# Kernel tuning notes

Measured on AMD Instinct MI355X. Metric: run time of the kernel, lower is better.

## Reference

```python
import jax, jax.numpy as jnp
import numpy as np

NUM_HEADS = 16

def setup_inputs() -> dict:
    key = jax.random.key(0)
    ks = jax.random.split(key, 6)
    B, N, E = 2, 2048, 2048
    QK, V, M = 2048, 2048, 4096
    x = jax.random.normal(ks[0], (B, N, E), dtype=jnp.float32)
    Wq = jax.random.normal(ks[1], (QK, E), dtype=jnp.float32) * 0.02
    k_weight = jax.random.normal(ks[2], (M, QK), dtype=jnp.float32) * 0.05
    v_weight = jax.random.normal(ks[3], (M, V), dtype=jnp.float32) * 0.05
    Wg = jax.random.normal(ks[4], (V, E), dtype=jnp.float32) * 0.02
    Wout = jax.random.normal(ks[5], (E, V), dtype=jnp.float32) * 0.02
    return {"x": x, "Wq": Wq, "k_weight": k_weight, "v_weight": v_weight, "Wg": Wg, "Wout": Wout}

def reference(x, Wq, k_weight, v_weight, Wg, Wout):
    H = NUM_HEADS
    B, N, E = x.shape
    M = k_weight.shape[0]
    # q: [B, N, QK] -> [B, H, N, dk]
    q = jnp.einsum('bne,fe->bnf', x, Wq)
    dk = q.shape[-1] // H
    q = q.reshape(B, N, H, dk).transpose(0, 2, 1, 3)
    # k: [M, QK] -> [H, M, dk]; v: [M, V] -> [H, M, dv]
    k = k_weight.reshape(M, H, dk).transpose(1, 0, 2)
    dv = v_weight.shape[1] // H
    v = v_weight.reshape(M, H, dv).transpose(1, 0, 2)
    scale = jnp.asarray(dk, x.dtype) ** 0.5  # use_scale == 1
    k = k * scale
    v = v * scale
    # non-softmax attention over fixed memory
    energy = jax.nn.silu(jnp.einsum('bhnd,hmd->bhnm', q, k))  # [B,H,N,M]
    out = jnp.einsum('bhnm,hmd->bhnd', energy, v)  # [B,H,N,dv]
    out = out.transpose(0, 2, 1, 3).reshape(B, N, H * dv)
    # output gate (silu)
    gate = jax.nn.silu(jnp.einsum('bne,ve->bnv', x, Wg))
    out = out * gate
    return jnp.einsum('bnv,ev->bne', out, Wout)
```

## Files before the change

### kernel.cpp

```cpp
#include <hip/hip_runtime.h>

typedef __bf16 bf16;
typedef __bf16 bf16x4 __attribute__((ext_vector_type(4)));
typedef __bf16 bf16x8 __attribute__((ext_vector_type(8)));
typedef float f32x4 __attribute__((ext_vector_type(4)));

#define MFMA(a, b, c) __builtin_amdgcn_mfma_f32_16x16x32_bf16(a, b, c, 0, 0, 0)

__device__ __forceinline__ float fast_silu(float x) {
  float e = __builtin_amdgcn_exp2f(x * -1.4426950408889634f);
  return x * __builtin_amdgcn_rcpf(1.f + e);
}

__device__ __forceinline__ void gload_lds16(const void* g, void* l) {
  __builtin_amdgcn_global_load_lds(
      (const __attribute__((address_space(1))) void*)g,
      (__attribute__((address_space(3))) void*)l, 16, 0, 0);
}

__global__ __launch_bounds__(256) void cvt_bf16(const float* __restrict__ in,
                                                bf16* __restrict__ out, int n) {
  int i = (blockIdx.x * 256 + threadIdx.x) * 4;
  if (i >= n) return;
  float4 v = *(const float4*)(in + i);
  bf16x4 o = {(bf16)v.x, (bf16)v.y, (bf16)v.z, (bf16)v.w};
  *(bf16x4*)(out + i) = o;
}

__global__ __launch_bounds__(256) void transpose_v_cvt(const float* __restrict__ v,
                                                       bf16* __restrict__ vt) {
  __shared__ bf16 T[64 * 72];
  const int m0 = blockIdx.x * 64, c0 = blockIdx.y * 64;
  const int tid = threadIdx.x;
  const int tr = tid >> 3;
  const int tc = (tid & 7) << 3;
#pragma unroll
  for (int it = 0; it < 2; it++) {
    int r = tr + it * 32;
    const float* src = v + (long)(m0 + r) * 2048 + c0 + tc;
    float4 a = *(const float4*)src;
    float4 b = *(const float4*)(src + 4);
    bf16x8 t = {(bf16)a.x, (bf16)a.y, (bf16)a.z, (bf16)a.w,
                (bf16)b.x, (bf16)b.y, (bf16)b.z, (bf16)b.w};
    *(bf16x8*)&T[r * 72 + tc] = t;
  }
  __syncthreads();
#pragma unroll
  for (int it = 0; it < 2; it++) {
    int c = tr + it * 32;
    bf16x8 o;
#pragma unroll
    for (int j = 0; j < 8; j++) o[j] = T[(tc + j) * 72 + c];
    *(bf16x8*)(vt + (long)(c0 + c) * 4096 + m0 + tc) = o;
  }
}

template <int MODE>
__global__ __launch_bounds__(256, 2) void gemm_bt(const bf16* __restrict__ A,
                                                  const bf16* __restrict__ B,
                                                  const bf16* __restrict__ B2,
                                                  bf16* __restrict__ C1,
                                                  bf16* __restrict__ C2,
                                                  float* __restrict__ Cf, int M, int N, int K) {
  __shared__ bf16 As[128 * 32];
  __shared__ bf16 Bs[128 * 32];
  const int tid = threadIdx.x;
  const int wave = tid >> 6, lane = tid & 63;
  const int wr = wave >> 1, wc = wave & 1;
  const bool gsel = (MODE == 3) && (blockIdx.x >= 16);
  const bf16* Bm = gsel ? B2 : B;
  const long bM = (long)blockIdx.y * 128;
  const long bN = (long)((MODE == 3) ? (blockIdx.x & 15) : blockIdx.x) * 128;

  f32x4 acc[4][4] = {};

  const int srow = (wave << 5) + (lane >> 2);
  const int sg = ((lane & 3) ^ ((lane >> 3) & 3)) << 3;
  const bf16* Ag = A + (bM + srow) * (long)K + sg;
  const bf16* Bg = Bm + (bN + srow) * (long)K + sg;
  bf16* Asl = &As[srow * 32 + ((lane & 3) << 3)];
  bf16* Bsl = &Bs[srow * 32 + ((lane & 3) << 3)];

  const int fr = lane & 15;
  const int gofs = (((lane >> 4) ^ ((fr >> 1) & 3)) << 3);

  for (int k0 = 0; k0 < K; k0 += 32) {
    __syncthreads();
    gload_lds16(Ag + k0, Asl);
    gload_lds16(Ag + k0 + (long)16 * K, Asl + 16 * 32);
    gload_lds16(Bg + k0, Bsl);
    gload_lds16(Bg + k0 + (long)16 * K, Bsl + 16 * 32);
    __syncthreads();
    bf16x8 af[4], bfv[4];
#pragma unroll
    for (int i = 0; i < 4; i++)
      af[i] = *(const bf16x8*)&As[(wr * 64 + i * 16 + fr) * 32 + gofs];
#pragma unroll
    for (int j = 0; j < 4; j++)
      bfv[j] = *(const bf16x8*)&Bs[(wc * 64 + j * 16 + fr) * 32 + gofs];
#pragma unroll
    for (int i = 0; i < 4; i++)
#pragma unroll
      for (int j = 0; j < 4; j++) acc[i][j] = MFMA(af[i], bfv[j], acc[i][j]);
  }

  const int er = wr * 64 + ((lane >> 4) << 2);
  const int ec = wc * 64 + (lane & 15);
#pragma unroll
  for (int i = 0; i < 4; i++)
#pragma unroll
    for (int j = 0; j < 4; j++)
#pragma unroll
      for (int r = 0; r < 4; r++) {
        long row = bM + er + i * 16 + r;
        long col = bN + ec + j * 16;
        float v = acc[i][j][r];
        if (MODE == 2) {
          Cf[row * (long)N + col] = v;
        } else {
          if (gsel)
            C2[row * (long)N + col] = (bf16)fast_silu(v);
          else
            C1[row * (long)N + col] = (bf16)(v * 11.3137085f);
        }
      }
}

__global__ __launch_bounds__(256, 2) void attn_fused(const bf16* __restrict__ q,
                                                     const bf16* __restrict__ kw,
                                                     const bf16* __restrict__ vt,
                                                     bf16* __restrict__ gate_io) {
  constexpr int E = 2048, M = 4096;
  constexpr float scale = 11.3137085f;
  const int bid = blockIdx.x;
  const int h = ((bid & 7) << 1) | ((bid >> 8) & 1);
  const int sub = (bid >> 3) & 31;
  const int b = sub >> 4, nt = sub & 15;
  const long n0 = (long)b * 2048 + nt * 128;

  const int tid = threadIdx.x, wave = tid >> 6, lane = tid & 63;
  const int quad = lane >> 4, ln = lane & 15;
  const int sw_m = wave & 1, sw_n = wave >> 1;
  const int pw_n = wave & 1, pw_dv = wave >> 1;

  __shared__ bf16 Ks[64 * 128];
  __shared__ bf16 Vts[128 * 64];
  __shared__ bf16 Ps[128 * 64];

  const bf16* qbase = q + (n0 + sw_n * 64) * E + h * 128;
  bf16x8 qf[4][4];
#pragma unroll
  for (int n2 = 0; n2 < 4; n2++)
#pragma unroll
    for (int ks = 0; ks < 4; ks++)
      qf[n2][ks] = *(const bf16x8*)(qbase + (long)(n2 * 16 + ln) * E + ks * 32 + (quad << 3));

  f32x4 oacc[4][4] = {};

  const bf16* kg = kw + (long)((wave << 4) + quad) * E + h * 128;
  bf16* ksl = &Ks[(wave << 4) * 128 + lane * 8];
  int kc[4];
#pragma unroll
  for (int i = 0; i < 4; i++) kc[i] = (ln ^ ((quad + i * 4) & 15)) << 3;

  const bf16* vg = vt + (long)(h * 128 + (wave << 5) + (lane >> 3)) * M +
                   (((lane & 7) ^ ((lane >> 3) & 7)) << 3);
  bf16* vsl = &Vts[(wave << 5) * 64 + lane * 8];

  int waddr[2][4];
#pragma unroll
  for (int mt = 0; mt < 2; mt++)
#pragma unroll
    for (int n2 = 0; n2 < 4; n2++) {
      int n = sw_n * 64 + n2 * 16 + ln;
      int mb8 = sw_m * 4 + mt * 2 + (quad >> 1);
      waddr[mt][n2] = n * 64 + ((mb8 ^ (n & 7)) << 3) + ((quad & 1) << 2);
    }

  for (int m0 = 0; m0 < M; m0 += 64) {
    __syncthreads();
#pragma unroll
    for (int i = 0; i < 4; i++) {
      gload_lds16(kg + (long)(m0 + i * 4) * E + kc[i], ksl + i * 4 * 128);
      gload_lds16(vg + m0 + (long)i * 8 * M, vsl + i * 8 * 64);
    }
    __syncthreads();

    f32x4 sacc[2][4] = {};
#pragma unroll
    for (int ks = 0; ks < 4; ks++) {
      bf16x8 af[2];
#pragma unroll
      for (int mt = 0; mt < 2; mt++)
        af[mt] = *(const bf16x8*)&Ks[(sw_m * 32 + mt * 16 + ln) * 128 +
                                     (((ks * 4 + quad) ^ ln) << 3)];
#pragma unroll
      for (int mt = 0; mt < 2; mt++)
#pragma unroll
        for (int n2 = 0; n2 < 4; n2++) sacc[mt][n2] = MFMA(af[mt], qf[n2][ks], sacc[mt][n2]);
    }

#pragma unroll
    for (int mt = 0; mt < 2; mt++)
#pragma unroll
      for (int n2 = 0; n2 < 4; n2++) {
        bf16x4 p;
#pragma unroll
        for (int r = 0; r < 4; r++) p[r] = (bf16)fast_silu(sacc[mt][n2][r]);
        *(bf16x4*)&Ps[waddr[mt][n2]] = p;
      }
    __syncthreads();

#pragma unroll
    for (int ks = 0; ks < 2; ks++) {
      const int so = ((ks * 4 + quad) ^ (ln & 7)) << 3;
      bf16x8 pf[4], vf[4];
#pragma unroll
      for (int n2 = 0; n2 < 4; n2++)
        pf[n2] = *(const bf16x8*)&Ps[(pw_n * 64 + n2 * 16 + ln) * 64 + so];
#pragma unroll
      for (int dt = 0; dt < 4; dt++)
        vf[dt] = *(const bf16x8*)&Vts[(pw_dv * 64 + dt * 16 + ln) * 64 + so];
#pragma unroll
      for (int n2 = 0; n2 < 4; n2++)
#pragma unroll
        for (int dt = 0; dt < 4; dt++) oacc[n2][dt] = MFMA(pf[n2], vf[dt], oacc[n2][dt]);
    }
  }

  bf16* gio = gate_io + n0 * E + h * 128;
#pragma unroll
  for (int n2 = 0; n2 < 4; n2++)
#pragma unroll
    for (int dt = 0; dt < 4; dt++)
#pragma unroll
      for (int r = 0; r < 4; r++) {
        int n = pw_n * 64 + n2 * 16 + quad * 4 + r;
        int dv = pw_dv * 64 + dt * 16 + ln;
        float g = (float)gio[(long)n * E + dv];
        gio[(long)n * E + dv] = (bf16)(g * oacc[n2][dt][r] * scale);
      }
}

extern "C" void kernel_launch(void* const* d_in, const int* in_sizes, int n_in,
                              void* d_out, int out_size, void* d_ws, size_t ws_size,
                              hipStream_t stream) {
  const float* x = (const float*)d_in[0];
  const float* Wq = (const float*)d_in[1];
  const float* kw = (const float*)d_in[2];
  const float* vw = (const float*)d_in[3];
  const float* Wg = (const float*)d_in[4];
  const float* Wout = (const float*)d_in[5];
  float* out = (float*)d_out;
  bf16* ws = (bf16*)d_ws;

  bf16* S0 = ws;
  bf16* S1 = ws + 8388608;
  bf16* S2 = ws + 16777216;
  bf16* S3 = ws + 25165824;
  bf16* S4 = ws + 33554432;
  bf16* Wgb = S1 + 4194304;

  cvt_bf16<<<8192, 256, 0, stream>>>(x, S0, 8388608);
  cvt_bf16<<<4096, 256, 0, stream>>>(Wq, S1, 4194304);
  cvt_bf16<<<4096, 256, 0, stream>>>(Wg, Wgb, 4194304);
  transpose_v_cvt<<<dim3(64, 32), 256, 0, stream>>>(vw, S2);
  gemm_bt<3><<<dim3(32, 32), 256, 0, stream>>>(S0, S1, Wgb, S3, S4, (float*)nullptr, 4096, 2048,
                                               2048);
  cvt_bf16<<<8192, 256, 0, stream>>>(kw, S0, 8388608);
  attn_fused<<<512, 256, 0, stream>>>(S3, S0, S2, S4);
  cvt_bf16<<<4096, 256, 0, stream>>>(Wout, S1, 4194304);
  gemm_bt<2><<<dim3(16, 32), 256, 0, stream>>>(S4, S1, (const bf16*)nullptr, (bf16*)nullptr,
                                               (bf16*)nullptr, out, 4096, 2048, 2048);
}
```

Measured before the change: 478.1 us.

## Double-buffer K/V LDS tiles and prefetch next chunk during attention compute

Splits the K and V^T shared-memory tiles into two buffers so the async global-to-LDS loads for the next 64-row memory chunk are issued before computing on the current one. Replaces __syncthreads with explicit waitcnt plus barrier pairs and raises wave priority around the MFMA loops. The aim is to hide global load latency behind the matrix work, at the cost of doubling K/V LDS usage, which may reduce occupancy from the requested two blocks per CU.

```diff
diff --git a/kernel.cpp b/kernel.cpp
--- a/kernel.cpp
+++ b/kernel.cpp
@@ -143,8 +143,8 @@
   const int sw_m = wave & 1, sw_n = wave >> 1;
   const int pw_n = wave & 1, pw_dv = wave >> 1;
 
-  __shared__ bf16 Ks[64 * 128];
-  __shared__ bf16 Vts[128 * 64];
+  __shared__ bf16 Ks[2][64 * 128];
+  __shared__ bf16 Vts[2][128 * 64];
   __shared__ bf16 Ps[128 * 64];
 
   const bf16* qbase = q + (n0 + sw_n * 64) * E + h * 128;
@@ -158,14 +158,14 @@
   f32x4 oacc[4][4] = {};
 
   const bf16* kg = kw + (long)((wave << 4) + quad) * E + h * 128;
-  bf16* ksl = &Ks[(wave << 4) * 128 + lane * 8];
+  const int ksl_off = (wave << 4) * 128 + lane * 8;
   int kc[4];
 #pragma unroll
   for (int i = 0; i < 4; i++) kc[i] = (ln ^ ((quad + i * 4) & 15)) << 3;
 
   const bf16* vg = vt + (long)(h * 128 + (wave << 5) + (lane >> 3)) * M +
                    (((lane & 7) ^ ((lane >> 3) & 7)) << 3);
-  bf16* vsl = &Vts[(wave << 5) * 64 + lane * 8];
+  const int vsl_off = (wave << 5) * 64 + lane * 8;
 
   int waddr[2][4];
 #pragma unroll
@@ -177,28 +177,36 @@
       waddr[mt][n2] = n * 64 + ((mb8 ^ (n & 7)) << 3) + ((quad & 1) << 2);
     }
 
-  for (int m0 = 0; m0 < M; m0 += 64) {
-    __syncthreads();
+  auto stage = [&](int ms, int sb) {
 #pragma unroll
     for (int i = 0; i < 4; i++) {
-      gload_lds16(kg + (long)(m0 + i * 4) * E + kc[i], ksl + i * 4 * 128);
-      gload_lds16(vg + m0 + (long)i * 8 * M, vsl + i * 8 * 64);
-    }
-    __syncthreads();
+      gload_lds16(kg + (long)(ms + i * 4) * E + kc[i], &Ks[sb][ksl_off + i * 4 * 128]);
+      gload_lds16(vg + ms + (long)i * 8 * M, &Vts[sb][vsl_off + i * 8 * 64]);
+    }
+  };
+
+  stage(0, 0);
+  asm volatile("s_waitcnt vmcnt(0)" ::: "memory");
+  __builtin_amdgcn_s_barrier();
+
+  auto body = [&](int m0, int rb, int sb, bool doStage) {
+    if (doStage) stage(m0 + 64, sb);
 
     f32x4 sacc[2][4] = {};
+    __builtin_amdgcn_s_setprio(1);
 #pragma unroll
     for (int ks = 0; ks < 4; ks++) {
       bf16x8 af[2];
 #pragma unroll
       for (int mt = 0; mt < 2; mt++)
-        af[mt] = *(const bf16x8*)&Ks[(sw_m * 32 + mt * 16 + ln) * 128 +
-                                     (((ks * 4 + quad) ^ ln) << 3)];
+        af[mt] = *(const bf16x8*)&Ks[rb][(sw_m * 32 + mt * 16 + ln) * 128 +
+                                         (((ks * 4 + quad) ^ ln) << 3)];
 #pragma unroll
       for (int mt = 0; mt < 2; mt++)
 #pragma unroll
         for (int n2 = 0; n2 < 4; n2++) sacc[mt][n2] = MFMA(af[mt], qf[n2][ks], sacc[mt][n2]);
     }
+    __builtin_amdgcn_s_setprio(0);
 
 #pragma unroll
     for (int mt = 0; mt < 2; mt++)
@@ -209,7 +217,9 @@
         for (int r = 0; r < 4; r++) p[r] = (bf16)fast_silu(sacc[mt][n2][r]);
         *(bf16x4*)&Ps[waddr[mt][n2]] = p;
       }
-    __syncthreads();
+
+    asm volatile("s_waitcnt lgkmcnt(0)" ::: "memory");
+    __builtin_amdgcn_s_barrier();
 
 #pragma unroll
     for (int ks = 0; ks < 2; ks++) {
@@ -220,12 +230,22 @@
         pf[n2] = *(const bf16x8*)&Ps[(pw_n * 64 + n2 * 16 + ln) * 64 + so];
 #pragma unroll
       for (int dt = 0; dt < 4; dt++)
-        vf[dt] = *(const bf16x8*)&Vts[(pw_dv * 64 + dt * 16 + ln) * 64 + so];
+        vf[dt] = *(const bf16x8*)&Vts[rb][(pw_dv * 64 + dt * 16 + ln) * 64 + so];
+      __builtin_amdgcn_s_setprio(1);
 #pragma unroll
       for (int n2 = 0; n2 < 4; n2++)
 #pragma unroll
         for (int dt = 0; dt < 4; dt++) oacc[n2][dt] = MFMA(pf[n2], vf[dt], oacc[n2][dt]);
-    }
+      __builtin_amdgcn_s_setprio(0);
+    }
+
+    asm volatile("s_waitcnt vmcnt(0)" ::: "memory");
+    __builtin_amdgcn_s_barrier();
+  };
+
+  for (int m0 = 0; m0 < M; m0 += 128) {
+    body(m0, 0, 1, true);
+    body(m0 + 64, 1, 0, m0 + 128 < M);
   }
 
   bf16* gio = gate_io + n0 * E + h * 128;
```

Measured after the change: 500.8 us. +4.8%, slower.
